# Kernel tuning notes

Hardware: AMD Instinct MI355X
Metric: run time of the kernel (lower is better)

Reference implementation:

```python
import jax, jax.numpy as jnp
import numpy as np

B, N, M, HID = 8, 384, 1536, 384
LRELU = 0.3
EPS = 1e-5


def _conv1d(x, w, b):
    # x: (B, C_in, L), w: (C_out, C_in, 3), 'same' padding
    y = jax.lax.conv_general_dilated(x, w, window_strides=(1,), padding=[(1, 1)],
                                     dimension_numbers=('NCH', 'OIH', 'NCH'))
    return y + b[None, :, None]


def _layer_norm(x, g, b):
    mu = jnp.mean(x, -1, keepdims=True)
    var = jnp.mean((x - mu) ** 2, -1, keepdims=True)
    return (x - mu) * jax.lax.rsqrt(var + EPS) * g + b


def _mlp(x, w1, b1, w2, b2):
    x = jax.nn.silu(x @ w1.T + b1)
    return jax.nn.silu(x @ w2.T + b2)


def setup_inputs() -> dict:
    key = jax.random.key(0)
    it = iter(jax.random.split(key, 48))
    def rn(shape, s):
        return jax.random.normal(next(it), shape, jnp.float32) * s
    h = HID
    inp = {}
    inp['H'] = rn((B, N, h), 1.0)
    # padding mask: last 32 phoneme slots are padding
    inp['src_mask'] = jnp.broadcast_to(jnp.arange(N)[None, :] >= N - 32, (B, N))
    inp['n_frames'] = M
    for i in (1, 2, 3):
        inp[f'w_c{i}'] = rn((h, h, 3), (1.0 / (3 * h)) ** 0.5)
        inp[f'b_c{i}'] = jnp.zeros((h,), jnp.float32)
        inp[f'g_ln{i}'] = jnp.ones((h,), jnp.float32)
        inp[f'be_ln{i}'] = jnp.zeros((h,), jnp.float32)
    inp['w_dp'] = rn((1, h), h ** -0.5)
    inp['b_dp'] = jnp.zeros((1,), jnp.float32)
    inp['w_proj'] = rn((h, h), h ** -0.5)
    inp['b_proj'] = jnp.zeros((h,), jnp.float32)
    inp['w_conv'] = rn((8, h, 3), (1.0 / (3 * h)) ** 0.5)
    inp['b_conv'] = jnp.zeros((8,), jnp.float32)
    inp['g_gn'] = jnp.ones((8,), jnp.float32)
    inp['b_gn'] = jnp.zeros((8,), jnp.float32)
    inp['wq1'] = rn((10, 10), 0.3)
    inp['bq1'] = jnp.zeros((10,), jnp.float32)
    inp['wq2'] = rn((4, 10), 0.3)
    inp['bq2'] = jnp.zeros((4,), jnp.float32)
    inp['wp1'] = rn((10, 10), 0.3)
    inp['bp1'] = jnp.zeros((10,), jnp.float32)
    inp['wp2'] = rn((2, 10), 0.3)
    inp['bp2'] = jnp.zeros((2,), jnp.float32)
    inp['w_wh'] = rn((h, 4 * h), (4 * h) ** -0.5)
    inp['b_wh'] = jnp.zeros((h,), jnp.float32)
    inp['w_wc'] = rn((h, 8), 8 ** -0.5)
    inp['b_wc'] = jnp.zeros((h,), jnp.float32)
    return inp


def reference(H, src_mask, n_frames,
              w_c1, b_c1, g_ln1, be_ln1, w_c2, b_c2, g_ln2, be_ln2,
              w_c3, b_c3, g_ln3, be_ln3, w_dp, b_dp, w_proj, b_proj,
              w_conv, b_conv, g_gn, b_gn, wq1, bq1, wq2, bq2,
              wp1, bp1, wp2, bp2, w_wh, b_wh, w_wc, b_wc):
    b, n, h = H.shape
    m = n_frames
    # ---- DurationPredictor (3 conv blocks, dropout=eval/identity) ----
    x = H
    for (wc, bc, g, be) in ((w_c1, b_c1, g_ln1, be_ln1),
                            (w_c2, b_c2, g_ln2, be_ln2),
                            (w_c3, b_c3, g_ln3, be_ln3)):
        y = _conv1d(x.transpose(0, 2, 1), wc, bc)       # (b, h, n)
        y = jax.nn.leaky_relu(y, LRELU)
        x = _layer_norm(y.transpose(0, 2, 1), g, be)    # (b, n, h)
    d = x @ w_dp.T + b_dp                               # (b, n, 1)
    d = jnp.where(src_mask[..., None], 0.0, d)[..., 0]  # (b, n)
    # ---- duration matrices S, E (eq. 6) ----
    cs = jnp.cumsum(d, 1)                                # (b, n)
    i_s = jnp.arange(1, m + 1, dtype=H.dtype)[None, :, None]  # (1, m, 1)
    csp = jnp.concatenate([jnp.zeros((b, 1), d.dtype), cs], 1)[:, :-1]
    S = i_s - csp[:, None, :]                            # (b, m, n)
    E = cs[:, None, :] - i_s                             # (b, m, n)
    # ---- project: Conv1D(Proj(H)) + GroupNorm(1,8) + SiLU ----
    p = H @ w_proj.T + b_proj                            # (b, n, h)
    p = _conv1d(p.transpose(0, 2, 1), w_conv, b_conv)    # (b, 8, n)
    mu = jnp.mean(p, (1, 2), keepdims=True)
    var = jnp.mean((p - mu) ** 2, (1, 2), keepdims=True)
    p = (p - mu) * jax.lax.rsqrt(var + EPS) * g_gn[None, :, None] + b_gn[None, :, None]
    proj = jax.nn.silu(p).transpose(0, 2, 1)             # (b, n, 8)
    # ---- concat [S, E, proj] -> (b, m, n, 10) ----
    concat = jnp.concatenate([S[..., None], E[..., None],
                              jnp.broadcast_to(proj[:, None], (b, m, n, 8))], -1)
    C = _mlp(concat, wp1, bp1, wp2, bp2)                 # (b, m, n, 2)
    W = _mlp(concat, wq1, bq1, wq2, bq2)                 # (b, m, n, 4)
    W = jnp.where(src_mask[:, None, :, None], -1e9, W)
    W = jax.nn.softmax(W, axis=2)                        # softmax over n
    Wp = W.transpose(0, 3, 1, 2)                         # (b, q, m, n)
    O_left = jnp.einsum('bqmn,bnh->bmqh', Wp, H).reshape(b, m, -1) @ w_wh.T + b_wh
    O_right = jnp.einsum('bqmn,bmnp->bmqp', Wp, C).reshape(b, m, -1) @ w_wc.T + b_wc
    return O_left + O_right
```

## Files before the change

kernel.cpp:

```cpp
#include <hip/hip_runtime.h>

#define DI __device__ __forceinline__

typedef __attribute__((ext_vector_type(8))) short bf16x8;
typedef __attribute__((ext_vector_type(4))) float f32x4;
typedef unsigned int u32;
typedef unsigned short u16;

namespace {
constexpr int Bn = 8;
constexpr int Nn = 384;
constexpr int HID = 384;
constexpr int Mn = 1536;
constexpr int NMASK = Nn - 32;
constexpr float LRELU = 0.3f;
constexpr float EPSV = 1e-5f;
constexpr int XROW = 386;
constexpr int YSZ = 3072*HID;

DI u16 f2bf(float f){
  union { float f; u32 i; } c; c.f = f;
  u32 r = c.i + 0x7fffu + ((c.i >> 16) & 1u);
  return (u16)(r >> 16);
}
DI u32 pk2bf(float a, float b){ return (u32)f2bf(a) | ((u32)f2bf(b) << 16); }
DI float sig_r(float x){ return __builtin_amdgcn_rcpf(1.f + __expf(-x)); }
DI float silu_f(float x){ return x * sig_r(x); }

template<int NC>
DI void wred_sum(float (&v)[NC]){
  #pragma unroll
  for (int o = 32; o; o >>= 1)
    #pragma unroll
    for (int i = 0; i < NC; i++) v[i] += __shfl_xor(v[i], o);
}
template<int NC>
DI void wred_max(float (&v)[NC]){
  #pragma unroll
  for (int o = 32; o; o >>= 1)
    #pragma unroll
    for (int i = 0; i < NC; i++) v[i] = fmaxf(v[i], __shfl_xor(v[i], o));
}

DI void gload16(const u16* g, u16* lds){
  __builtin_amdgcn_global_load_lds((const __attribute__((address_space(1))) u32*)(g),
                                   (__attribute__((address_space(3))) u32*)(lds), 16, 0, 0);
}

DI void gemm_core(const u16* __restrict__ A, int ldA, const u16* __restrict__ BT, int ldB,
                  int KT, u16* As, u16* Bs, int lane, int wid, f32x4 (&acc)[4][4])
{
  const int wr = wid >> 1, wc = wid & 1;
  const int frow = lane & 15;
  const int fch  = lane >> 4;
  const int srow = wid*32 + (lane >> 3);
  const int sch  = lane & 7;
  for (int kt = 0; kt < KT; kt++){
    const int k0 = kt*64;
    #pragma unroll
    for (int i = 0; i < 4; i++){
      int row = srow + i*8;
      int gch = sch ^ (row & 7);
      gload16(A  + (size_t)row*ldA + k0 + gch*8, As + (wid*32 + i*8)*64);
      gload16(BT + (size_t)row*ldB + k0 + gch*8, Bs + (wid*32 + i*8)*64);
    }
    __syncthreads();
    bf16x8 af[2][4], bf[2][4];
    #pragma unroll
    for (int kh = 0; kh < 2; kh++){
      #pragma unroll
      for (int mi = 0; mi < 4; mi++){
        int r = wr*64 + mi*16 + frow;
        int slot = (kh*4 + fch) ^ (r & 7);
        af[kh][mi] = *(const bf16x8*)(As + r*64 + slot*8);
      }
      #pragma unroll
      for (int ni = 0; ni < 4; ni++){
        int r = wc*64 + ni*16 + frow;
        int slot = (kh*4 + fch) ^ (r & 7);
        bf[kh][ni] = *(const bf16x8*)(Bs + r*64 + slot*8);
      }
    }
    #pragma unroll
    for (int kh = 0; kh < 2; kh++)
      #pragma unroll
      for (int mi = 0; mi < 4; mi++)
        #pragma unroll
        for (int ni = 0; ni < 4; ni++)
          acc[mi][ni] = __builtin_amdgcn_mfma_f32_16x16x32_bf16(af[kh][mi], bf[kh][ni], acc[mi][ni], 0, 0, 0);
    __syncthreads();
  }
}
}

__global__ __launch_bounds__(256) void prep_all(
    const float* __restrict__ w1, const float* __restrict__ w2, const float* __restrict__ w3,
    const float* __restrict__ wconv, const float* __restrict__ w_wh,
    const float* __restrict__ w_proj, const float* __restrict__ H,
    u16* __restrict__ wkT, float* __restrict__ wconvT, u16* __restrict__ Wcat,
    u16* __restrict__ xpad1, u16* __restrict__ xpad2)
{
  int g = blockIdx.x*256 + threadIdx.x;
  const int S0 = 3*HID*HID;
  if (g < S0){
    int l = g / (HID*HID);
    int r = g % (HID*HID);
    const float* w = (l==0) ? w1 : ((l==1) ? w2 : w3);
    float a = w[r*3+0], b = w[r*3+1], c = w[r*3+2];
    u16* base = wkT + (size_t)l*3*HID*HID + r;
    base[0]         = f2bf(a);
    base[HID*HID]   = f2bf(b);
    base[2*HID*HID] = f2bf(c);
    return;
  }
  g -= S0;
  const int S1 = 8*HID;
  if (g < S1){
    int c = g / HID, ci = g % HID;
    const float* src = wconv + ((size_t)c*HID + ci)*3;
    wconvT[(c*3+0)*HID + ci] = src[0];
    wconvT[(c*3+1)*HID + ci] = src[1];
    wconvT[(c*3+2)*HID + ci] = src[2];
    return;
  }
  g -= S1;
  const int S2 = 1920*HID/4;
  if (g < S2){
    int e0 = g*4;
    int n = e0 / HID, kk = e0 % HID;
    float4 v;
    if (n < 1536){
      int q = n / HID, h = n % HID;
      v = *(const float4*)(w_wh + (size_t)h*1536 + q*HID + kk);
    } else {
      v = *(const float4*)(w_proj + (size_t)(n-1536)*HID + kk);
    }
    *(ushort4*)(Wcat + e0) = make_ushort4(f2bf(v.x), f2bf(v.y), f2bf(v.z), f2bf(v.w));
    return;
  }
  g -= S2;
  const int S3 = Bn*XROW*(HID/4);
  if (g < S3){
    int b = g / (XROW*96);
    int r = g % (XROW*96);
    int row = r / 96, c4 = r % 96;
    ushort4 o = make_ushort4(0,0,0,0);
    if (row >= 1 && row <= Nn){
      float4 v = *(const float4*)(H + (((size_t)b*Nn) + row - 1)*HID + c4*4);
      o = make_ushort4(f2bf(v.x), f2bf(v.y), f2bf(v.z), f2bf(v.w));
    }
    *(ushort4*)(xpad1 + ((size_t)b*XROW + row)*HID + c4*4) = o;
    return;
  }
  g -= S3;
  if (g < Bn*2*96){
    int b = g / (2*96);
    int r = g % (2*96);
    int row = (r / 96) ? (XROW-1) : 0;
    int c4 = r % 96;
    *(ushort4*)(xpad2 + ((size_t)b*XROW + row)*HID + c4*4) = make_ushort4(0,0,0,0);
  }
}

__global__ __launch_bounds__(256) void conv_mfma(
    const u16* __restrict__ xpad, const u16* __restrict__ wkT, float* __restrict__ ys)
{
  __shared__ u16 As[128*64];
  __shared__ u16 Bs[128*64];
  const int t = threadIdx.x, lane = t & 63, wid = t >> 6;
  const int mt = blockIdx.x;
  const int nt = blockIdx.y;
  const int kz = blockIdx.z;
  const int b = mt / 3, jt = mt % 3;
  float* y = ys + (size_t)kz*YSZ;
  f32x4 acc[4][4];
  #pragma unroll
  for (int i = 0; i < 4; i++)
    #pragma unroll
    for (int jj = 0; jj < 4; jj++) acc[i][jj] = f32x4{0.f,0.f,0.f,0.f};
  gemm_core(xpad + ((size_t)b*XROW + jt*128 + kz)*HID, HID,
            wkT + (size_t)kz*HID*HID + (size_t)nt*128*HID, HID, HID/64,
            As, Bs, lane, wid, acc);
  const int wr = wid >> 1, wc = wid & 1;
  const int r0 = jt*128 + wr*64 + (lane >> 4)*4;
  const int c0 = nt*128 + wc*64 + (lane & 15);
  #pragma unroll
  for (int mi = 0; mi < 4; mi++)
    #pragma unroll
    for (int ni = 0; ni < 4; ni++)
      #pragma unroll
      for (int r = 0; r < 4; r++)
        y[((size_t)b*Nn + r0 + mi*16 + r)*HID + c0 + ni*16] = acc[mi][ni][r];
}

__global__ __launch_bounds__(256) void ln_row_kern(
    const float* __restrict__ ys, const float* __restrict__ bc, const float* __restrict__ g,
    const float* __restrict__ be, u16* __restrict__ xpad_out,
    const float* __restrict__ w_dp, const float* __restrict__ b_dp, float* __restrict__ d_out)
{
  const int row = (blockIdx.x*256 + threadIdx.x) >> 6;
  const int lane = threadIdx.x & 63;
  const int b = row / Nn, n = row % Nn;
  const int c0 = lane*6;
  const float* rp = ys + (size_t)row*HID + c0;
  float v[6] = {0.f,0.f,0.f,0.f,0.f,0.f};
  #pragma unroll
  for (int sl = 0; sl < 3; sl++){
    const float* p = rp + (size_t)sl*YSZ;
    float2 a0 = *(const float2*)(p);
    float2 a1 = *(const float2*)(p + 2);
    float2 a2 = *(const float2*)(p + 4);
    v[0]+=a0.x; v[1]+=a0.y; v[2]+=a1.x; v[3]+=a1.y; v[4]+=a2.x; v[5]+=a2.y;
  }
  #pragma unroll
  for (int e = 0; e < 6; e++){
    float x = v[e] + bc[c0+e];
    v[e] = x >= 0.f ? x : LRELU*x;
  }
  float s2[2] = {0.f, 0.f};
  #pragma unroll
  for (int e = 0; e < 6; e++){ s2[0] += v[e]; s2[1] += v[e]*v[e]; }
  wred_sum<2>(s2);
  const float mu = s2[0] * (1.f/HID);
  const float var = s2[1] * (1.f/HID) - mu*mu;
  const float rs = rsqrtf(var + EPSV);
  #pragma unroll
  for (int e = 0; e < 6; e++) v[e] = (v[e] - mu)*rs*g[c0+e] + be[c0+e];
  if (xpad_out){
    u32* dst = (u32*)(xpad_out + ((size_t)b*XROW + 1 + n)*HID + c0);
    dst[0] = pk2bf(v[0], v[1]);
    dst[1] = pk2bf(v[2], v[3]);
    dst[2] = pk2bf(v[4], v[5]);
  }
  if (d_out){
    float dv[1] = {0.f};
    #pragma unroll
    for (int e = 0; e < 6; e++) dv[0] += v[e]*w_dp[c0+e];
    wred_sum<1>(dv);
    if (lane == 0) d_out[row] = (n >= NMASK) ? 0.f : dv[0] + b_dp[0];
  }
}

__global__ __launch_bounds__(256) void hproj_mfma(
    const u16* __restrict__ xpad1, const u16* __restrict__ Wcat,
    const float* __restrict__ b_proj, u16* __restrict__ KtT, float* __restrict__ p1)
{
  __shared__ u16 As[128*64];
  __shared__ u16 Bs[128*64];
  const int t = threadIdx.x, lane = t & 63, wid = t >> 6;
  const int mt = blockIdx.x;
  const int nt = blockIdx.y;
  const int b = mt / 3, jt = mt % 3;
  f32x4 acc[4][4];
  #pragma unroll
  for (int i = 0; i < 4; i++)
    #pragma unroll
    for (int jj = 0; jj < 4; jj++) acc[i][jj] = f32x4{0.f,0.f,0.f,0.f};
  gemm_core(xpad1 + ((size_t)b*XROW + 1 + jt*128)*HID, HID,
            Wcat + (size_t)nt*128*HID, HID, HID/64, As, Bs, lane, wid, acc);
  const int wr = wid >> 1, wc = wid & 1;
  const int j0 = jt*128 + wr*64 + (lane >> 4)*4;
  if (nt < 12){
    const int q = nt / 3;
    const int hb = (nt % 3)*128 + wc*64 + (lane & 15);
    #pragma unroll
    for (int mi = 0; mi < 4; mi++){
      #pragma unroll
      for (int ni = 0; ni < 4; ni++){
        int h = hb + ni*16;
        int j = j0 + mi*16;
        ushort4 pk = make_ushort4(f2bf(acc[mi][ni][0]), f2bf(acc[mi][ni][1]),
                                  f2bf(acc[mi][ni][2]), f2bf(acc[mi][ni][3]));
        *(ushort4*)(KtT + (size_t)b*589824 + (size_t)h*1536 + q*HID + j) = pk;
      }
    }
  } else {
    const int hb = (nt - 12)*128 + wc*64 + (lane & 15);
    #pragma unroll
    for (int mi = 0; mi < 4; mi++){
      #pragma unroll
      for (int ni = 0; ni < 4; ni++){
        int h = hb + ni*16;
        float bp = b_proj[h];
        #pragma unroll
        for (int r = 0; r < 4; r++){
          int j = j0 + mi*16 + r;
          p1[((size_t)b*Nn + j)*HID + h] = acc[mi][ni][r] + bp;
        }
      }
    }
  }
}

__global__ __launch_bounds__(256) void projc8_kern(
    const float* __restrict__ p1, const float* __restrict__ wconvT,
    const float* __restrict__ b_conv, float* __restrict__ p8tmp, float* __restrict__ partials)
{
  __shared__ float xs[34][388];
  __shared__ float sc[8];
  const int b  = blockIdx.x / 12;
  const int ch = blockIdx.x % 12;
  const int n0 = ch*32;
  const int t  = threadIdx.x;
  for (int idx = t; idx < 34*96; idx += 256){
    int r = idx / 96, c4 = idx % 96;
    int n = n0 - 1 + r;
    float4 v = (n >= 0 && n < Nn) ? *(const float4*)(p1 + ((size_t)b*Nn + n)*HID + c4*4)
                                  : make_float4(0.f,0.f,0.f,0.f);
    *(float4*)(&xs[r][c4*4]) = v;
  }
  __syncthreads();
  const int nl = t >> 3, c = t & 7;
  const float* wb = wconvT + (size_t)c*3*HID;
  float pc = b_conv[c];
  for (int ci = 0; ci < HID; ci += 4){
    float4 w0 = *(const float4*)(wb + ci);
    float4 w1 = *(const float4*)(wb + HID + ci);
    float4 w2 = *(const float4*)(wb + 2*HID + ci);
    float4 x0 = *(const float4*)(&xs[nl][ci]);
    float4 x1 = *(const float4*)(&xs[nl+1][ci]);
    float4 x2 = *(const float4*)(&xs[nl+2][ci]);
    pc += w0.x*x0.x + w0.y*x0.y + w0.z*x0.z + w0.w*x0.w
        + w1.x*x1.x + w1.y*x1.y + w1.z*x1.z + w1.w*x1.w
        + w2.x*x2.x + w2.y*x2.y + w2.z*x2.z + w2.w*x2.w;
  }
  p8tmp[((size_t)b*Nn + n0 + nl)*8 + c] = pc;
  float sv[2] = {pc, pc*pc};
  #pragma unroll
  for (int o = 32; o; o >>= 1){ sv[0] += __shfl_down(sv[0], o); sv[1] += __shfl_down(sv[1], o); }
  if ((t & 63) == 0){ sc[(t>>6)*2] = sv[0]; sc[(t>>6)*2+1] = sv[1]; }
  __syncthreads();
  if (t == 0){
    float s = 0.f, q = 0.f;
    #pragma unroll
    for (int w = 0; w < 4; w++){ s += sc[w*2]; q += sc[w*2+1]; }
    partials[blockIdx.x*2] = s; partials[blockIdx.x*2+1] = q;
  }
}

__global__ __launch_bounds__(Nn) void gnwprep_kern(
    const float* __restrict__ p8tmp, const float* __restrict__ partials,
    const float* __restrict__ g_gn, const float* __restrict__ b_gn,
    const float* __restrict__ d,
    const float* __restrict__ wq1, const float* __restrict__ bq1,
    const float* __restrict__ wp1, const float* __restrict__ bp1,
    float* __restrict__ baseQP)
{
  __shared__ float sb[Nn];
  const int b = blockIdx.x, j = threadIdx.x;
  const float dj = d[b*Nn + j];
  float incl = dj;
  sb[j] = incl;
  __syncthreads();
  for (int off = 1; off < Nn; off <<= 1){
    float add = (j >= off) ? sb[j - off] : 0.f;
    __syncthreads();
    incl += add;
    sb[j] = incl;
    __syncthreads();
  }
  const float csj = incl;
  const float csp = incl - dj;
  float s = 0.f, q = 0.f;
  #pragma unroll
  for (int i = 0; i < 12; i++){ s += partials[(b*12+i)*2]; q += partials[(b*12+i)*2+1]; }
  const float inv = 1.f/(8.f*Nn);
  const float mu = s*inv;
  const float var = q*inv - mu*mu;
  const float rs = rsqrtf(var + EPSV);
  float4 v0 = *(const float4*)(p8tmp + ((size_t)b*Nn + j)*8);
  float4 v1 = *(const float4*)(p8tmp + ((size_t)b*Nn + j)*8 + 4);
  float p8[8] = {v0.x,v0.y,v0.z,v0.w,v1.x,v1.y,v1.z,v1.w};
  #pragma unroll
  for (int c = 0; c < 8; c++) p8[c] = silu_f((p8[c]-mu)*rs*g_gn[c] + b_gn[c]);
  #pragma unroll
  for (int i = 0; i < 10; i++){
    float v = bq1[i] - wq1[i*10+0]*csp + wq1[i*10+1]*csj;
    float u = bp1[i] - wp1[i*10+0]*csp + wp1[i*10+1]*csj;
    #pragma unroll
    for (int k = 0; k < 8; k++){
      v += wq1[i*10+2+k]*p8[k];
      u += wp1[i*10+2+k]*p8[k];
    }
    baseQP[((size_t)b*20 + i)*Nn + j]      = v;
    baseQP[((size_t)b*20 + 10 + i)*Nn + j] = u;
  }
}

__global__ __launch_bounds__(512) void wsoft_kern(
    const float* __restrict__ baseQP,
    const float* __restrict__ wq1, const float* __restrict__ wq2, const float* __restrict__ bq2,
    const float* __restrict__ wp1, const float* __restrict__ wp2, const float* __restrict__ bp2,
    u16* __restrict__ Wt, float* __restrict__ R)
{
  __shared__ float bs[20*Nn];
  const int t = threadIdx.x, lane = t & 63, wid = t >> 6;
  const int g = blockIdx.x*8 + wid;
  const int bb = (blockIdx.x*8) / Mn;
  const int m = g - bb*Mn;
  for (int idx = t; idx < 20*Nn/4; idx += 512)
    *(float4*)(&bs[idx*4]) = *(const float4*)(baseQP + (size_t)bb*20*Nn + idx*4);
  __syncthreads();
  const float fi = (float)(m + 1);
  float w4s[6][4], c2s[6][2];
  #pragma unroll
  for (int s = 0; s < 6; s++){
    const int j = s*64 + lane;
    float h1[10];
    #pragma unroll
    for (int i = 0; i < 10; i++){
      float sl = wq1[i*10+0] - wq1[i*10+1];
      h1[i] = silu_f(fmaf(sl, fi, bs[i*Nn + j]));
    }
    const bool masked = (s == 5) && (lane >= 32);
    #pragma unroll
    for (int o = 0; o < 4; o++){
      float v = bq2[o];
      #pragma unroll
      for (int k = 0; k < 10; k++) v += wq2[o*10+k]*h1[k];
      w4s[s][o] = masked ? -1e9f : silu_f(v);
    }
    #pragma unroll
    for (int i = 0; i < 10; i++){
      float sl = wp1[i*10+0] - wp1[i*10+1];
      h1[i] = silu_f(fmaf(sl, fi, bs[(10+i)*Nn + j]));
    }
    #pragma unroll
    for (int o = 0; o < 2; o++){
      float v = bp2[o];
      #pragma unroll
      for (int k = 0; k < 10; k++) v += wp2[o*10+k]*h1[k];
      c2s[s][o] = silu_f(v);
    }
  }
  float mx[4] = {-3e38f,-3e38f,-3e38f,-3e38f};
  #pragma unroll
  for (int s = 0; s < 6; s++)
    #pragma unroll
    for (int o = 0; o < 4; o++) mx[o] = fmaxf(mx[o], w4s[s][o]);
  wred_max<4>(mx);
  float sm[4] = {0.f,0.f,0.f,0.f};
  #pragma unroll
  for (int s = 0; s < 6; s++)
    #pragma unroll
    for (int o = 0; o < 4; o++){ w4s[s][o] = __expf(w4s[s][o] - mx[o]); sm[o] += w4s[s][o]; }
  wred_sum<4>(sm);
  float inv[4];
  #pragma unroll
  for (int o = 0; o < 4; o++) inv[o] = __builtin_amdgcn_rcpf(sm[o]);
  float pr[8] = {0.f,0.f,0.f,0.f,0.f,0.f,0.f,0.f};
  #pragma unroll
  for (int s = 0; s < 6; s++){
    const int j = s*64 + lane;
    #pragma unroll
    for (int o = 0; o < 4; o++){
      float wn = w4s[s][o]*inv[o];
      Wt[(size_t)g*1536 + o*Nn + j] = f2bf(wn);
      pr[o*2+0] += wn*c2s[s][0];
      pr[o*2+1] += wn*c2s[s][1];
    }
  }
  wred_sum<8>(pr);
  if (lane == 0){
    #pragma unroll
    for (int i = 0; i < 8; i++) R[(size_t)g*8 + i] = pr[i];
  }
}

__global__ __launch_bounds__(256) void outgemm_mfma(
    const u16* __restrict__ Wt, const u16* __restrict__ KtT,
    const float* __restrict__ R, const float* __restrict__ b_wh,
    const float* __restrict__ w_wc, const float* __restrict__ b_wc,
    float* __restrict__ out)
{
  __shared__ u16 As[128*64];
  __shared__ u16 Bs[128*64];
  const int t = threadIdx.x, lane = t & 63, wid = t >> 6;
  const int mt = blockIdx.x;
  const int nt = blockIdx.y;
  const int b  = blockIdx.z;
  f32x4 acc[4][4];
  #pragma unroll
  for (int i = 0; i < 4; i++)
    #pragma unroll
    for (int jj = 0; jj < 4; jj++) acc[i][jj] = f32x4{0.f,0.f,0.f,0.f};
  gemm_core(Wt + (size_t)b*Mn*1536 + (size_t)mt*128*1536, 1536,
            KtT + (size_t)b*589824 + (size_t)nt*128*1536, 1536, 24,
            As, Bs, lane, wid, acc);
  const int wr = wid >> 1, wc = wid & 1;
  float bbv[4], wcv[4][8];
  #pragma unroll
  for (int ni = 0; ni < 4; ni++){
    int h = nt*128 + wc*64 + ni*16 + (lane & 15);
    bbv[ni] = b_wh[h] + b_wc[h];
    float4 a0 = *(const float4*)(w_wc + (size_t)h*8);
    float4 a1 = *(const float4*)(w_wc + (size_t)h*8 + 4);
    wcv[ni][0]=a0.x; wcv[ni][1]=a0.y; wcv[ni][2]=a0.z; wcv[ni][3]=a0.w;
    wcv[ni][4]=a1.x; wcv[ni][5]=a1.y; wcv[ni][6]=a1.z; wcv[ni][7]=a1.w;
  }
  #pragma unroll
  for (int mi = 0; mi < 4; mi++){
    #pragma unroll
    for (int r = 0; r < 4; r++){
      int m = mt*128 + wr*64 + mi*16 + (lane >> 4)*4 + r;
      const float* Rp = R + ((size_t)b*Mn + m)*8;
      float4 r0 = *(const float4*)(Rp);
      float4 r1 = *(const float4*)(Rp + 4);
      float R8[8] = {r0.x,r0.y,r0.z,r0.w,r1.x,r1.y,r1.z,r1.w};
      #pragma unroll
      for (int ni = 0; ni < 4; ni++){
        int h = nt*128 + wc*64 + ni*16 + (lane & 15);
        float v = acc[mi][ni][r] + bbv[ni];
        #pragma unroll
        for (int p = 0; p < 8; p++) v += R8[p]*wcv[ni][p];
        out[((size_t)b*Mn + m)*HID + h] = v;
      }
    }
  }
}

extern "C" void kernel_launch(void* const* d_in, const int* in_sizes, int n_in,
                              void* d_out, int out_size, void* d_ws, size_t ws_size,
                              hipStream_t stream) {
  (void)in_sizes; (void)n_in; (void)out_size; (void)ws_size;
  const float* Hin    = (const float*)d_in[0];
  const float* w_c1   = (const float*)d_in[3];
  const float* b_c1   = (const float*)d_in[4];
  const float* g1     = (const float*)d_in[5];
  const float* be1    = (const float*)d_in[6];
  const float* w_c2   = (const float*)d_in[7];
  const float* b_c2   = (const float*)d_in[8];
  const float* g2     = (const float*)d_in[9];
  const float* be2    = (const float*)d_in[10];
  const float* w_c3   = (const float*)d_in[11];
  const float* b_c3   = (const float*)d_in[12];
  const float* g3     = (const float*)d_in[13];
  const float* be3    = (const float*)d_in[14];
  const float* w_dp   = (const float*)d_in[15];
  const float* b_dp   = (const float*)d_in[16];
  const float* w_proj = (const float*)d_in[17];
  const float* b_proj = (const float*)d_in[18];
  const float* w_conv = (const float*)d_in[19];
  const float* b_conv = (const float*)d_in[20];
  const float* g_gn   = (const float*)d_in[21];
  const float* b_gn   = (const float*)d_in[22];
  const float* wq1    = (const float*)d_in[23];
  const float* bq1    = (const float*)d_in[24];
  const float* wq2    = (const float*)d_in[25];
  const float* bq2    = (const float*)d_in[26];
  const float* wp1    = (const float*)d_in[27];
  const float* bp1    = (const float*)d_in[28];
  const float* wp2    = (const float*)d_in[29];
  const float* bp2    = (const float*)d_in[30];
  const float* w_wh   = (const float*)d_in[31];
  const float* b_wh   = (const float*)d_in[32];
  const float* w_wc   = (const float*)d_in[33];
  const float* b_wc   = (const float*)d_in[34];

  char* ws = (char*)d_ws;
  u16*   Wt      = (u16*)(ws + 0);
  u16*   wkT     = (u16*)(ws + 0);
  float* wconvT  = (float*)(ws + 2654208);
  u16*   Wcat    = (u16*)(ws + 2691072);
  float* ys      = (float*)(ws + 4194304);
  u16*   KtT     = (u16*)(ws + 37748736);
  u16*   xpad1   = (u16*)(ws + 47185920);
  float* baseQP  = (float*)(ws + 47185920);
  u16*   xpad2   = (u16*)(ws + 49557504);
  float* R_w     = (float*)(ws + 49557504);
  float* p1      = (float*)(ws + 51929088);
  float* p8tmp   = (float*)(ws + 56647680);
  float* partials= (float*)(ws + 56745984);
  float* d_w     = (float*)(ws + 56747008);

  const int PREP_T = 3*HID*HID + 8*HID + 1920*HID/4 + Bn*XROW*(HID/4) + Bn*2*(HID/4);
  prep_all<<<(PREP_T + 255)/256, 256, 0, stream>>>(w_c1, w_c2, w_c3, w_conv, w_wh, w_proj, Hin,
                                                   wkT, wconvT, Wcat, xpad1, xpad2);

  conv_mfma<<<dim3(24,3,3), 256, 0, stream>>>(xpad1, wkT,             ys);
  ln_row_kern<<<Bn*Nn/4, 256, 0, stream>>>(ys, b_c1, g1, be1, xpad2, nullptr, nullptr, nullptr);
  conv_mfma<<<dim3(24,3,3), 256, 0, stream>>>(xpad2, wkT + 3*HID*HID, ys);
  ln_row_kern<<<Bn*Nn/4, 256, 0, stream>>>(ys, b_c2, g2, be2, xpad2, nullptr, nullptr, nullptr);
  conv_mfma<<<dim3(24,3,3), 256, 0, stream>>>(xpad2, wkT + 6*HID*HID, ys);
  ln_row_kern<<<Bn*Nn/4, 256, 0, stream>>>(ys, b_c3, g3, be3, nullptr, w_dp, b_dp, d_w);

  hproj_mfma<<<dim3(24,15), 256, 0, stream>>>(xpad1, Wcat, b_proj, KtT, p1);

  projc8_kern<<<Bn*12, 256, 0, stream>>>(p1, wconvT, b_conv, p8tmp, partials);
  gnwprep_kern<<<Bn, Nn, 0, stream>>>(p8tmp, partials, g_gn, b_gn, d_w, wq1, bq1, wp1, bp1, baseQP);

  wsoft_kern<<<Bn*Mn/8, 512, 0, stream>>>(baseQP, wq1, wq2, bq2, wp1, wp2, bp2, Wt, R_w);

  outgemm_mfma<<<dim3(12,3,8), 256, 0, stream>>>(Wt, KtT, R_w, b_wh, w_wc, b_wc, (float*)d_out);
}
```

Before: 204.9 us.

## Merge independent kernels into combined launches to fill the GPU

Merges the first conv GEMM and the H-projection GEMM into one launch with a combined grid (216 + 360 blocks). Also merges the third layer-norm/duration reduction with the 8-channel projection conv into one launch selected by block index. The two pairs are independent, so this removes two launches and lets small grids that underfill the device run side by side. The cost is more register and LDS pressure per block from the unified kernels and branch-divergent block roles.

```diff
diff --git a/kernel.cpp b/kernel.cpp
--- a/kernel.cpp
+++ b/kernel.cpp
@@ -162,6 +162,76 @@
   }
 }
 
+__global__ __launch_bounds__(256) void c1hp_mfma(
+    const u16* __restrict__ xpad1, const u16* __restrict__ wkT, float* __restrict__ ys,
+    const u16* __restrict__ Wcat, const float* __restrict__ b_proj,
+    u16* __restrict__ KtT, float* __restrict__ p1)
+{
+  __shared__ u16 As[128*64];
+  __shared__ u16 Bs[128*64];
+  const int t = threadIdx.x, lane = t & 63, wid = t >> 6;
+  const int mt = blockIdx.x;
+  const int yb = blockIdx.y;
+  const int b = mt / 3, jt = mt % 3;
+  f32x4 acc[4][4];
+  #pragma unroll
+  for (int i = 0; i < 4; i++)
+    #pragma unroll
+    for (int jj = 0; jj < 4; jj++) acc[i][jj] = f32x4{0.f,0.f,0.f,0.f};
+  const int wr = wid >> 1, wc = wid & 1;
+  if (yb < 9){
+    const int nt = yb / 3, kz = yb % 3;
+    gemm_core(xpad1 + ((size_t)b*XROW + jt*128 + kz)*HID, HID,
+              wkT + (size_t)kz*HID*HID + (size_t)nt*128*HID, HID, HID/64,
+              As, Bs, lane, wid, acc);
+    float* y = ys + (size_t)kz*YSZ;
+    const int r0 = jt*128 + wr*64 + (lane >> 4)*4;
+    const int c0 = nt*128 + wc*64 + (lane & 15);
+    #pragma unroll
+    for (int mi = 0; mi < 4; mi++)
+      #pragma unroll
+      for (int ni = 0; ni < 4; ni++)
+        #pragma unroll
+        for (int r = 0; r < 4; r++)
+          y[((size_t)b*Nn + r0 + mi*16 + r)*HID + c0 + ni*16] = acc[mi][ni][r];
+  } else {
+    const int nt = yb - 9;
+    gemm_core(xpad1 + ((size_t)b*XROW + 1 + jt*128)*HID, HID,
+              Wcat + (size_t)nt*128*HID, HID, HID/64, As, Bs, lane, wid, acc);
+    const int j0 = jt*128 + wr*64 + (lane >> 4)*4;
+    if (nt < 12){
+      const int q = nt / 3;
+      const int hb = (nt % 3)*128 + wc*64 + (lane & 15);
+      #pragma unroll
+      for (int mi = 0; mi < 4; mi++){
+        #pragma unroll
+        for (int ni = 0; ni < 4; ni++){
+          int h = hb + ni*16;
+          int j = j0 + mi*16;
+          ushort4 pk = make_ushort4(f2bf(acc[mi][ni][0]), f2bf(acc[mi][ni][1]),
+                                    f2bf(acc[mi][ni][2]), f2bf(acc[mi][ni][3]));
+          *(ushort4*)(KtT + (size_t)b*589824 + (size_t)h*1536 + q*HID + j) = pk;
+        }
+      }
+    } else {
+      const int hb = (nt - 12)*128 + wc*64 + (lane & 15);
+      #pragma unroll
+      for (int mi = 0; mi < 4; mi++){
+        #pragma unroll
+        for (int ni = 0; ni < 4; ni++){
+          int h = hb + ni*16;
+          float bp = b_proj[h];
+          #pragma unroll
+          for (int r = 0; r < 4; r++){
+            int j = j0 + mi*16 + r;
+            p1[((size_t)b*Nn + j)*HID + h] = acc[mi][ni][r] + bp;
+          }
+        }
+      }
+    }
+  }
+}
+
 __global__ __launch_bounds__(256) void conv_mfma(
     const u16* __restrict__ xpad, const u16* __restrict__ wkT, float* __restrict__ ys)
 {
@@ -241,100 +311,87 @@
   }
 }
 
-__global__ __launch_bounds__(256) void hproj_mfma(
-    const u16* __restrict__ xpad1, const u16* __restrict__ Wcat,
-    const float* __restrict__ b_proj, u16* __restrict__ KtT, float* __restrict__ p1)
-{
-  __shared__ u16 As[128*64];
-  __shared__ u16 Bs[128*64];
-  const int t = threadIdx.x, lane = t & 63, wid = t >> 6;
-  const int mt = blockIdx.x;
-  const int nt = blockIdx.y;
-  const int b = mt / 3, jt = mt % 3;
-  f32x4 acc[4][4];
-  #pragma unroll
-  for (int i = 0; i < 4; i++)
-    #pragma unroll
-    for (int jj = 0; jj < 4; jj++) acc[i][jj] = f32x4{0.f,0.f,0.f,0.f};
-  gemm_core(xpad1 + ((size_t)b*XROW + 1 + jt*128)*HID, HID,
-            Wcat + (size_t)nt*128*HID, HID, HID/64, As, Bs, lane, wid, acc);
-  const int wr = wid >> 1, wc = wid & 1;
-  const int j0 = jt*128 + wr*64 + (lane >> 4)*4;
-  if (nt < 12){
-    const int q = nt / 3;
-    const int hb = (nt % 3)*128 + wc*64 + (lane & 15);
-    #pragma unroll
-    for (int mi = 0; mi < 4; mi++){
-      #pragma unroll
-      for (int ni = 0; ni < 4; ni++){
-        int h = hb + ni*16;
-        int j = j0 + mi*16;
-        ushort4 pk = make_ushort4(f2bf(acc[mi][ni][0]), f2bf(acc[mi][ni][1]),
-                                  f2bf(acc[mi][ni][2]), f2bf(acc[mi][ni][3]));
-        *(ushort4*)(KtT + (size_t)b*589824 + (size_t)h*1536 + q*HID + j) = pk;
-      }
-    }
-  } else {
-    const int hb = (nt - 12)*128 + wc*64 + (lane & 15);
-    #pragma unroll
-    for (int mi = 0; mi < 4; mi++){
-      #pragma unroll
-      for (int ni = 0; ni < 4; ni++){
-        int h = hb + ni*16;
-        float bp = b_proj[h];
-        #pragma unroll
-        for (int r = 0; r < 4; r++){
-          int j = j0 + mi*16 + r;
-          p1[((size_t)b*Nn + j)*HID + h] = acc[mi][ni][r] + bp;
-        }
-      }
-    }
-  }
-}
-
-__global__ __launch_bounds__(256) void projc8_kern(
+__global__ __launch_bounds__(256) void ln3pc8_kern(
+    const float* __restrict__ ys, const float* __restrict__ bc, const float* __restrict__ g,
+    const float* __restrict__ be, const float* __restrict__ w_dp,
+    const float* __restrict__ b_dp, float* __restrict__ d_out,
     const float* __restrict__ p1, const float* __restrict__ wconvT,
     const float* __restrict__ b_conv, float* __restrict__ p8tmp, float* __restrict__ partials)
 {
   __shared__ float xs[34][388];
   __shared__ float sc[8];
-  const int b  = blockIdx.x / 12;
-  const int ch = blockIdx.x % 12;
-  const int n0 = ch*32;
-  const int t  = threadIdx.x;
-  for (int idx = t; idx < 34*96; idx += 256){
-    int r = idx / 96, c4 = idx % 96;
-    int n = n0 - 1 + r;
-    float4 v = (n >= 0 && n < Nn) ? *(const float4*)(p1 + ((size_t)b*Nn + n)*HID + c4*4)
-                                  : make_float4(0.f,0.f,0.f,0.f);
-    *(float4*)(&xs[r][c4*4]) = v;
-  }
-  __syncthreads();
-  const int nl = t >> 3, c = t & 7;
-  const float* wb = wconvT + (size_t)c*3*HID;
-  float pc = b_conv[c];
-  for (int ci = 0; ci < HID; ci += 4){
-    float4 w0 = *(const float4*)(wb + ci);
-    float4 w1 = *(const float4*)(wb + HID + ci);
-    float4 w2 = *(const float4*)(wb + 2*HID + ci);
-    float4 x0 = *(const float4*)(&xs[nl][ci]);
-    float4 x1 = *(const float4*)(&xs[nl+1][ci]);
-    float4 x2 = *(const float4*)(&xs[nl+2][ci]);
-    pc += w0.x*x0.x + w0.y*x0.y + w0.z*x0.z + w0.w*x0.w
-        + w1.x*x1.x + w1.y*x1.y + w1.z*x1.z + w1.w*x1.w
-        + w2.x*x2.x + w2.y*x2.y + w2.z*x2.z + w2.w*x2.w;
-  }
-  p8tmp[((size_t)b*Nn + n0 + nl)*8 + c] = pc;
-  float sv[2] = {pc, pc*pc};
-  #pragma unroll
-  for (int o = 32; o; o >>= 1){ sv[0] += __shfl_down(sv[0], o); sv[1] += __shfl_down(sv[1], o); }
-  if ((t & 63) == 0){ sc[(t>>6)*2] = sv[0]; sc[(t>>6)*2+1] = sv[1]; }
-  __syncthreads();
-  if (t == 0){
-    float s = 0.f, q = 0.f;
-    #pragma unroll
-    for (int w = 0; w < 4; w++){ s += sc[w*2]; q += sc[w*2+1]; }
-    partials[blockIdx.x*2] = s; partials[blockIdx.x*2+1] = q;
+  if (blockIdx.x < 768){
+    const int row = (blockIdx.x*256 + threadIdx.x) >> 6;
+    const int lane = threadIdx.x & 63;
+    const int n = row % Nn;
+    const int c0 = lane*6;
+    const float* rp = ys + (size_t)row*HID + c0;
+    float v[6] = {0.f,0.f,0.f,0.f,0.f,0.f};
+    #pragma unroll
+    for (int sl = 0; sl < 3; sl++){
+      const float* p = rp + (size_t)sl*YSZ;
+      float2 a0 = *(const float2*)(p);
+      float2 a1 = *(const float2*)(p + 2);
+      float2 a2 = *(const float2*)(p + 4);
+      v[0]+=a0.x; v[1]+=a0.y; v[2]+=a1.x; v[3]+=a1.y; v[4]+=a2.x; v[5]+=a2.y;
+    }
+    #pragma unroll
+    for (int e = 0; e < 6; e++){
+      float x = v[e] + bc[c0+e];
+      v[e] = x >= 0.f ? x : LRELU*x;
+    }
+    float s2[2] = {0.f, 0.f};
+    #pragma unroll
+    for (int e = 0; e < 6; e++){ s2[0] += v[e]; s2[1] += v[e]*v[e]; }
+    wred_sum<2>(s2);
+    const float mu = s2[0] * (1.f/HID);
+    const float var = s2[1] * (1.f/HID) - mu*mu;
+    const float rs = rsqrtf(var + EPSV);
+    float dv[1] = {0.f};
+    #pragma unroll
+    for (int e = 0; e < 6; e++) dv[0] += ((v[e]-mu)*rs*g[c0+e] + be[c0+e])*w_dp[c0+e];
+    wred_sum<1>(dv);
+    if (lane == 0) d_out[row] = (n >= NMASK) ? 0.f : dv[0] + b_dp[0];
+  } else {
+    const int bid = blockIdx.x - 768;
+    const int b  = bid / 12;
+    const int ch = bid % 12;
+    const int n0 = ch*32;
+    const int t  = threadIdx.x;
+    for (int idx = t; idx < 34*96; idx += 256){
+      int r = idx / 96, c4 = idx % 96;
+      int n = n0 - 1 + r;
+      float4 v = (n >= 0 && n < Nn) ? *(const float4*)(p1 + ((size_t)b*Nn + n)*HID + c4*4)
+                                    : make_float4(0.f,0.f,0.f,0.f);
+      *(float4*)(&xs[r][c4*4]) = v;
+    }
+    __syncthreads();
+    const int nl = t >> 3, c = t & 7;
+    const float* wb = wconvT + (size_t)c*3*HID;
+    float pc = b_conv[c];
+    for (int ci = 0; ci < HID; ci += 4){
+      float4 w0 = *(const float4*)(wb + ci);
+      float4 w1 = *(const float4*)(wb + HID + ci);
+      float4 w2 = *(const float4*)(wb + 2*HID + ci);
+      float4 x0 = *(const float4*)(&xs[nl][ci]);
+      float4 x1 = *(const float4*)(&xs[nl+1][ci]);
+      float4 x2 = *(const float4*)(&xs[nl+2][ci]);
+      pc += w0.x*x0.x + w0.y*x0.y + w0.z*x0.z + w0.w*x0.w
+          + w1.x*x1.x + w1.y*x1.y + w1.z*x1.z + w1.w*x1.w
+          + w2.x*x2.x + w2.y*x2.y + w2.z*x2.z + w2.w*x2.w;
+    }
+    p8tmp[((size_t)b*Nn + n0 + nl)*8 + c] = pc;
+    float sv[2] = {pc, pc*pc};
+    #pragma unroll
+    for (int o = 32; o; o >>= 1){ sv[0] += __shfl_down(sv[0], o); sv[1] += __shfl_down(sv[1], o); }
+    if ((t & 63) == 0){ sc[(t>>6)*2] = sv[0]; sc[(t>>6)*2+1] = sv[1]; }
+    __syncthreads();
+    if (t == 0){
+      float s = 0.f, q = 0.f;
+      #pragma unroll
+      for (int w = 0; w < 4; w++){ s += sc[w*2]; q += sc[w*2+1]; }
+      partials[bid*2] = s; partials[bid*2+1] = q;
+    }
   }
 }
 
@@ -577,16 +634,14 @@
   prep_all<<<(PREP_T + 255)/256, 256, 0, stream>>>(w_c1, w_c2, w_c3, w_conv, w_wh, w_proj, Hin,
                                                    wkT, wconvT, Wcat, xpad1, xpad2);
 
-  conv_mfma<<<dim3(24,3,3), 256, 0, stream>>>(xpad1, wkT,             ys);
+  c1hp_mfma<<<dim3(24,24), 256, 0, stream>>>(xpad1, wkT, ys, Wcat, b_proj, KtT, p1);
   ln_row_kern<<<Bn*Nn/4, 256, 0, stream>>>(ys, b_c1, g1, be1, xpad2, nullptr, nullptr, nullptr);
   conv_mfma<<<dim3(24,3,3), 256, 0, stream>>>(xpad2, wkT + 3*HID*HID, ys);
   ln_row_kern<<<Bn*Nn/4, 256, 0, stream>>>(ys, b_c2, g2, be2, xpad2, nullptr, nullptr, nullptr);
   conv_mfma<<<dim3(24,3,3), 256, 0, stream>>>(xpad2, wkT + 6*HID*HID, ys);
-  ln_row_kern<<<Bn*Nn/4, 256, 0, stream>>>(ys, b_c3, g3, be3, nullptr, w_dp, b_dp, d_w);
-
-  hproj_mfma<<<dim3(24,15), 256, 0, stream>>>(xpad1, Wcat, b_proj, KtT, p1);
-
-  projc8_kern<<<Bn*12, 256, 0, stream>>>(p1, wconvT, b_conv, p8tmp, partials);
+
+  ln3pc8_kern<<<Bn*Nn/4 + Bn*12, 256, 0, stream>>>(ys, b_c3, g3, be3, w_dp, b_dp, d_w,
+                                                   p1, wconvT, b_conv, p8tmp, partials);
   gnwprep_kern<<<Bn, Nn, 0, stream>>>(p8tmp, partials, g_gn, b_gn, d_w, wq1, bq1, wp1, bp1, baseQP);
 
   wsoft_kern<<<Bn*Mn/8, 512, 0, stream>>>(baseQP, wq1, wq2, bq2, wp1, wp2, bp2, Wt, R_w);
```

Measured after the change: 237.7 us. 16.0% more time.
